# Optimization experiments

Measured on AMD Instinct MI355X. Metric: run time of the kernel, lower is better.

Reference implementation:

```python
import jax, jax.numpy as jnp
import numpy as np

V = 12000; WE = 1000; FEAT = 2048; FE = 1024; H = 1024; AH = 512; NREG = 36; B = 128; T = 17
PAD_ID = 0


def _lstm_cell(x, h, c, wih, whh, bih, bhh):
    # torch LSTMCell: gates ordered (input, forget, cell, output)
    g = x @ wih.T + h @ whh.T + bih + bhh
    i, f, gg, o = jnp.split(g, 4, axis=-1)
    c_new = jax.nn.sigmoid(f) * c + jax.nn.sigmoid(i) * jnp.tanh(gg)
    h_new = jax.nn.sigmoid(o) * jnp.tanh(c_new)
    return h_new, c_new


def setup_inputs() -> dict:
    key = jax.random.key(0)
    ks = jax.random.split(key, 24)
    s = 0.02
    emb_w = jax.random.normal(ks[0], (V, WE), jnp.float32) * s
    emb_w = emb_w.at[PAD_ID].set(0.0)  # padding_idx row is zero
    inp = {
        'fc_feats': jax.random.normal(ks[1], (B, FEAT), jnp.float32),
        'att_feats': jax.random.normal(ks[2], (B, NREG, FEAT), jnp.float32),
        'captions': jax.random.randint(ks[3], (B, T), 0, V, jnp.int64),
        'emb_w': emb_w,
        'fc_w': jax.random.normal(ks[4], (FEAT, FE), jnp.float32) * s,
        'fc_b': jnp.zeros((FE,), jnp.float32),
        'atte_w': jax.random.normal(ks[5], (FEAT, FE), jnp.float32) * s,
        'atte_b': jnp.zeros((FE,), jnp.float32),
        'ctx_w': jax.random.normal(ks[6], (FE, AH), jnp.float32) * s,
        'ctx_b': jnp.zeros((AH,), jnp.float32),
        'attl_wih': jax.random.normal(ks[7], (4 * H, H + FE + WE), jnp.float32) * s,
        'attl_whh': jax.random.normal(ks[8], (4 * H, H), jnp.float32) * s,
        'attl_bih': jnp.zeros((4 * H,), jnp.float32),
        'attl_bhh': jnp.zeros((4 * H,), jnp.float32),
        'h2att_w': jax.random.normal(ks[9], (H, AH), jnp.float32) * s,
        'h2att_b': jnp.zeros((AH,), jnp.float32),
        'alpha_w': jax.random.normal(ks[10], (AH,), jnp.float32) * s,
        'alpha_b': jnp.zeros((), jnp.float32),
        'langl_wih': jax.random.normal(ks[11], (4 * H, FE + H), jnp.float32) * s,
        'langl_whh': jax.random.normal(ks[12], (4 * H, H), jnp.float32) * s,
        'langl_bih': jnp.zeros((4 * H,), jnp.float32),
        'langl_bhh': jnp.zeros((4 * H,), jnp.float32),
        'cls_w': jax.random.normal(ks[13], (H, V), jnp.float32) * s,
        'cls_b': jnp.zeros((V,), jnp.float32),
    }
    return inp


def _forward(fc_feats, att_feats, captions, emb_w, fc_w, fc_b, atte_w, atte_b,
             ctx_w, ctx_b, attl_wih, attl_whh, attl_bih, attl_bhh,
             h2att_w, h2att_b, alpha_w, alpha_b,
             langl_wih, langl_whh, langl_bih, langl_bhh, cls_w, cls_b):
    # _prepare_features (eval mode: dropout is identity)
    fc_e = jax.nn.relu(fc_feats @ fc_w + fc_b)                 # [B, FE]
    att_e = jax.nn.relu(att_feats @ atte_w + atte_b)           # [B, N, FE]
    p_att = att_e @ ctx_w + ctx_b                              # [B, N, AH]
    bsz = fc_feats.shape[0]
    h0 = jnp.zeros((bsz, H), fc_feats.dtype)

    def step(carry, it):
        h_att, c_att, h_lang, c_lang = carry
        w = jax.nn.relu(emb_w[it])                             # [B, WE]
        x_att = jnp.concatenate([h_lang, fc_e, w], axis=1)
        h_att, c_att = _lstm_cell(x_att, h_att, c_att, attl_wih, attl_whh, attl_bih, attl_bhh)
        # Attention
        hq = h_att @ h2att_w + h2att_b                          # [B, AH]
        e = jnp.tanh(p_att + hq[:, None, :]) @ alpha_w + alpha_b  # [B, N]
        alpha = jax.nn.softmax(e, axis=1)
        att_res = jnp.einsum('bn,bnd->bd', alpha, att_e)        # [B, FE]
        x_lang = jnp.concatenate([att_res, h_att], axis=1)
        h_lang, c_lang = _lstm_cell(x_lang, h_lang, c_lang, langl_wih, langl_whh, langl_bih, langl_bhh)
        logprobs = jax.nn.log_softmax(h_lang @ cls_w + cls_b, axis=1)  # [B, V]
        return (h_att, c_att, h_lang, c_lang), logprobs

    its = captions[:, :-1].T  # [T-1, B]
    _, outs = jax.lax.scan(step, (h0, h0, h0, h0), its)
    return jnp.transpose(outs, (1, 0, 2))  # [B, T-1, V]


def reference(fc_feats, att_feats, captions, emb_w, fc_w, fc_b, atte_w, atte_b,
              ctx_w, ctx_b, attl_wih, attl_whh, attl_bih, attl_bhh,
              h2att_w, h2att_b, alpha_w, alpha_b,
              langl_wih, langl_whh, langl_bih, langl_bhh, cls_w, cls_b):
    return _forward(fc_feats, att_feats, captions, emb_w, fc_w, fc_b, atte_w, atte_b,
                    ctx_w, ctx_b, attl_wih, attl_whh, attl_bih, attl_bhh,
                    h2att_w, h2att_b, alpha_w, alpha_b,
                    langl_wih, langl_whh, langl_bih, langl_bhh, cls_w, cls_b)
```

## Files before the change

### kernel.cpp

```cpp
#include <hip/hip_runtime.h>
#include <cstddef>
#include <cstdint>

constexpr int CV    = 12000;
constexpr int CVP2  = 12288;
constexpr int CWE   = 1000;
constexpr int CFEAT = 2048;
constexpr int CFE   = 1024;
constexpr int CH    = 1024;
constexpr int CAH   = 512;
constexpr int CNREG = 36;
constexpr int CB    = 128;
constexpr int CT    = 17;
constexpr int G4    = 4096;
constexpr int XH    = 2048;
constexpr int XL3   = 3072;

#define CDIV(a,b) (((a)+(b)-1)/(b))

typedef __bf16 bf16_t;
typedef __bf16 bf16x8 __attribute__((ext_vector_type(8)));
typedef __bf16 bf16x4 __attribute__((ext_vector_type(4)));
typedef float  f32x4  __attribute__((ext_vector_type(4)));

typedef __attribute__((address_space(3))) uint32_t lds_u32;
typedef const __attribute__((address_space(1))) uint32_t glb_u32;

struct Seg { const bf16_t* A; const bf16_t* W; int lda, ldw, kt; };

template<bool RELU, bool OUTBF, int SWZ>
__global__ __launch_bounds__(256)
void pre_gemm(Seg s0, int inner, const float* __restrict__ bias1,
              void* __restrict__ Cout, int ldc)
{
    const int tid = threadIdx.x;
    const int wid = tid >> 6, lane = tid & 63;
    const int wr = wid >> 1, wc = wid & 1;
    const int llo = lane & 15, lhi = lane >> 4;
    const int nb = gridDim.x, id = blockIdx.x;
    const int sw = (id & 7) * (nb >> 3) + (id >> 3);
    int m0, n0;
    if (SWZ == 1)      { n0 = (sw / inner) * 64;  m0 = (sw % inner) * 128; }
    else if (SWZ == 2) { m0 = (sw / inner) * 128; n0 = (sw % inner) * 64;  }
    else {
        const int xcd = id & 7, idx = id >> 3;
        m0 = (((xcd >> 2) << 3) + (idx & 7)) * 128;
        n0 = (((xcd & 3) << 4) + (idx >> 3)) * 64;
    }

    __shared__ __align__(16) uint8_t smA[2][8192];
    __shared__ __align__(16) uint8_t smB[2][4096];

    const int TT = s0.kt;
    f32x4 acc[4][2] = {};

    const int scq = (lane & 3) ^ ((lane >> 3) & 3);
    auto stage = [&](int buf, int ti) {
        const int k0 = ti << 5;
        #pragma unroll
        for (int i = 0; i < 2; ++i) {
            const int cq = wid * 64 + lane + i * 256;
            const int row = cq >> 2;
            const bf16_t* ga = s0.A + (size_t)(m0 + row) * s0.lda + k0 + scq * 8;
            __builtin_amdgcn_global_load_lds((glb_u32*)ga,
                (lds_u32*)(smA[buf] + (wid * 64 + i * 256) * 16 + lane * 16), 16, 0, 0);
        }
        {
            const int row = tid >> 2;
            const bf16_t* gb = s0.W + (size_t)(n0 + row) * s0.ldw + k0 + scq * 8;
            __builtin_amdgcn_global_load_lds((glb_u32*)gb,
                (lds_u32*)(smB[buf] + wid * 1024 + lane * 16), 16, 0, 0);
        }
    };
    auto compute = [&](int buf) {
        bf16x8 af[4], bg[2];
        #pragma unroll
        for (int fm = 0; fm < 4; ++fm) {
            const int r = wr * 64 + fm * 16 + llo;
            const int p = lhi ^ ((r >> 1) & 3);
            af[fm] = *(const bf16x8*)(smA[buf] + r * 64 + p * 16);
        }
        #pragma unroll
        for (int fn = 0; fn < 2; ++fn) {
            const int r = wc * 32 + fn * 16 + llo;
            const int p = lhi ^ ((r >> 1) & 3);
            bg[fn] = *(const bf16x8*)(smB[buf] + r * 64 + p * 16);
        }
        #pragma unroll
        for (int fm = 0; fm < 4; ++fm)
            #pragma unroll
            for (int fn = 0; fn < 2; ++fn)
                acc[fm][fn] = __builtin_amdgcn_mfma_f32_16x16x32_bf16(
                    af[fm], bg[fn], acc[fm][fn], 0, 0, 0);
    };

    stage(0, 0);
    __syncthreads();
    int cur = 0;
    for (int ti = 0; ti < TT; ++ti) {
        if (ti + 1 < TT) stage(cur ^ 1, ti + 1);
        compute(cur);
        __syncthreads();
        cur ^= 1;
    }

    if (OUTBF) {
        bf16_t* st = (bf16_t*)smA;
        #pragma unroll
        for (int fn = 0; fn < 2; ++fn) {
            const int lcol = wc * 32 + fn * 16 + llo;
            const float b = bias1 ? bias1[n0 + lcol] : 0.f;
            #pragma unroll
            for (int fm = 0; fm < 4; ++fm)
                #pragma unroll
                for (int r = 0; r < 4; ++r) {
                    float v = acc[fm][fn][r] + b;
                    if (RELU) v = fmaxf(v, 0.f);
                    st[(wr * 64 + fm * 16 + lhi * 4 + r) * 64 + lcol] = (bf16_t)v;
                }
        }
        __syncthreads();
        #pragma unroll
        for (int i = 0; i < 4; ++i) {
            const int q = tid + i * 256;
            const int row = q >> 3, ch = q & 7;
            *(uint4*)((bf16_t*)Cout + (size_t)(m0 + row) * ldc + n0 + ch * 8)
                = *(const uint4*)&st[row * 64 + ch * 8];
        }
    } else {
        const int colb = n0 + wc * 32;
        const int rowb = m0 + wr * 64 + lhi * 4;
        #pragma unroll
        for (int fn = 0; fn < 2; ++fn) {
            const int col = colb + fn * 16 + llo;
            const float b = bias1 ? bias1[col] : 0.f;
            #pragma unroll
            for (int fm = 0; fm < 4; ++fm)
                #pragma unroll
                for (int r = 0; r < 4; ++r) {
                    float v = acc[fm][fn][r] + b;
                    if (RELU) v = fmaxf(v, 0.f);
                    ((float*)Cout)[(size_t)(rowb + fm * 16 + r) * ldc + col] = v;
                }
        }
    }
}

__global__ __launch_bounds__(256)
void cls_gemm(const bf16_t* __restrict__ A, const bf16_t* __restrict__ W,
              const float* __restrict__ bias, bf16_t* __restrict__ Cout)
{
    const int tid = threadIdx.x;
    const int wid = tid >> 6, lane = tid & 63;
    const int wr = wid >> 1, wc = wid & 1;
    const int llo = lane & 15, lhi = lane >> 4;
    const int id = blockIdx.x;
    const int xcd = id & 7, idx = id >> 3;
    const int mg = xcd & 1, ng = xcd >> 1;
    const int m0 = (mg * 8 + (idx & 7)) * 128;
    const int n0 = (ng * 24 + (idx >> 3)) * 128;

    __shared__ __align__(16) uint8_t smA[2][8192];
    __shared__ __align__(16) uint8_t smB[2][8192];

    constexpr int TT = 32;
    f32x4 acc[4][4] = {};

    const int scq = (lane & 3) ^ ((lane >> 3) & 3);
    auto stage = [&](int buf, int ti) {
        const int k0 = ti << 5;
        #pragma unroll
        for (int i = 0; i < 2; ++i) {
            const int cq = wid * 64 + lane + i * 256;
            const int row = cq >> 2;
            const bf16_t* ga = A + (size_t)(m0 + row) * CH + k0 + scq * 8;
            __builtin_amdgcn_global_load_lds((glb_u32*)ga,
                (lds_u32*)(smA[buf] + (wid * 64 + i * 256) * 16 + lane * 16), 16, 0, 0);
            const bf16_t* gb = W + (size_t)(n0 + row) * CH + k0 + scq * 8;
            __builtin_amdgcn_global_load_lds((glb_u32*)gb,
                (lds_u32*)(smB[buf] + (wid * 64 + i * 256) * 16 + lane * 16), 16, 0, 0);
        }
    };
    auto compute = [&](int buf) {
        bf16x8 af[4], bg[4];
        #pragma unroll
        for (int fm = 0; fm < 4; ++fm) {
            const int r = wr * 64 + fm * 16 + llo;
            const int p = lhi ^ ((r >> 1) & 3);
            af[fm] = *(const bf16x8*)(smA[buf] + r * 64 + p * 16);
        }
        #pragma unroll
        for (int fn = 0; fn < 4; ++fn) {
            const int r = wc * 64 + fn * 16 + llo;
            const int p = lhi ^ ((r >> 1) & 3);
            bg[fn] = *(const bf16x8*)(smB[buf] + r * 64 + p * 16);
        }
        #pragma unroll
        for (int fm = 0; fm < 4; ++fm)
            #pragma unroll
            for (int fn = 0; fn < 4; ++fn)
                acc[fm][fn] = __builtin_amdgcn_mfma_f32_16x16x32_bf16(
                    af[fm], bg[fn], acc[fm][fn], 0, 0, 0);
    };

    stage(0, 0);
    __syncthreads();
    int cur = 0;
    for (int ti = 0; ti < TT; ++ti) {
        if (ti + 1 < TT) stage(cur ^ 1, ti + 1);
        compute(cur);
        __syncthreads();
        cur ^= 1;
    }

    bf16_t* st = (bf16_t*)smA;
    #pragma unroll
    for (int fn = 0; fn < 4; ++fn) {
        const int lcol = wc * 64 + fn * 16 + llo;
        const int col = n0 + lcol;
        const float b = (col < CV) ? bias[col] : 0.f;
        #pragma unroll
        for (int fm = 0; fm < 4; ++fm)
            #pragma unroll
            for (int r = 0; r < 4; ++r)
                st[(wr * 64 + fm * 16 + lhi * 4 + r) * 128 + lcol]
                    = (bf16_t)(acc[fm][fn][r] + b);
    }
    __syncthreads();
    #pragma unroll
    for (int i = 0; i < 8; ++i) {
        const int q = tid + i * 256;
        const int row = q >> 4, ch = q & 15;
        *(uint4*)(Cout + (size_t)(m0 + row) * CVP2 + n0 + ch * 8)
            = *(const uint4*)&st[row * 128 + ch * 8];
    }
}

template<int TAG>
__global__ __launch_bounds__(256)
void gate_split(const bf16_t* __restrict__ A, int lda,
                const bf16_t* __restrict__ W, int ldw, int ktz,
                bf16_t* __restrict__ gpart)
{
    const int tid = threadIdx.x;
    const int w = tid >> 6, lane = tid & 63;
    const int llo = lane & 15, lhi = lane >> 4;
    const int n0 = blockIdx.x * 16;
    const int z  = blockIdx.y;
    const int kb = z * ktz;

    __shared__ __align__(16) uint8_t smA[2][16384];
    __shared__ __align__(16) uint8_t smB[2][2048];

    f32x4 acc0 = {0.f,0.f,0.f,0.f}, acc1 = {0.f,0.f,0.f,0.f};

    const int arow = tid >> 3, ac = tid & 7;
    const int asc = ac ^ (arow & 7);
    const int wvoff = (tid >> 6) * 1024;

    auto stage = [&](int buf, int ti) {
        const int k0 = (kb + ti) << 6;
        #pragma unroll
        for (int i = 0; i < 4; ++i) {
            const bf16_t* gp = A + (size_t)(arow + i * 32) * lda + k0 + asc * 8;
            __builtin_amdgcn_global_load_lds((glb_u32*)gp,
                (lds_u32*)(smA[buf] + i * 4096 + wvoff), 16, 0, 0);
        }
        if (tid < 128) {
            const int brow = tid >> 3, bc = tid & 7;
            const int bsc = bc ^ (brow & 7);
            const bf16_t* gp = W + (size_t)(n0 + brow) * ldw + k0 + bsc * 8;
            __builtin_amdgcn_global_load_lds((glb_u32*)gp,
                (lds_u32*)(smB[buf] + wvoff), 16, 0, 0);
        }
    };
    auto compute = [&](int buf) {
        const int r7 = llo & 7;
        #pragma unroll
        for (int kk = 0; kk < 2; ++kk) {
            const int coff = ((kk * 4 + lhi) ^ r7) << 4;
            bf16x8 a0 = *(const bf16x8*)(smA[buf] + (w * 32 + llo) * 128 + coff);
            bf16x8 a1 = *(const bf16x8*)(smA[buf] + (w * 32 + 16 + llo) * 128 + coff);
            bf16x8 bb = *(const bf16x8*)(smB[buf] + llo * 128 + coff);
            acc0 = __builtin_amdgcn_mfma_f32_16x16x32_bf16(a0, bb, acc0, 0, 0, 0);
            acc1 = __builtin_amdgcn_mfma_f32_16x16x32_bf16(a1, bb, acc1, 0, 0, 0);
        }
    };

    stage(0, 0);
    __syncthreads();
    int cur = 0;
    for (int ti = 0; ti < ktz; ++ti) {
        if (ti + 1 < ktz) stage(cur ^ 1, ti + 1);
        compute(cur);
        __syncthreads();
        cur ^= 1;
    }

    bf16_t* gp = gpart + (size_t)z * CB * G4;
    const int col = n0 + llo;
    #pragma unroll
    for (int r = 0; r < 4; ++r) {
        gp[(size_t)(w * 32 + lhi * 4 + r) * G4 + col] = (bf16_t)acc0[r];
        gp[(size_t)(w * 32 + 16 + lhi * 4 + r) * G4 + col] = (bf16_t)acc1[r];
    }
}

__global__ __launch_bounds__(1024)
void lstm_attn(const bf16_t* __restrict__ gpart, const bf16_t* __restrict__ gpre_fc,
               const bf16_t* __restrict__ gemb,
               const float* __restrict__ cbias, float* __restrict__ c_att,
               const bf16_t* __restrict__ p_att, const bf16_t* __restrict__ att_e,
               const bf16_t* __restrict__ h2att_wT, const float* __restrict__ h2att_b,
               const float* __restrict__ alpha_w, const float* __restrict__ alpha_b,
               bf16_t* __restrict__ xh_nxt, bf16_t* __restrict__ xl_cur)
{
    __shared__ float sh[CH];
    __shared__ float shq[CAH];
    __shared__ float se[64], salpha[64];
    const int b = blockIdx.x, tid = threadIdx.x;

    {
        const int j = tid;
        float g0 = 0.f, g1 = 0.f, g2 = 0.f, g3 = 0.f;
        #pragma unroll
        for (int z = 0; z < 4; ++z) {
            bf16x4 g = *(const bf16x4*)(gpart + (size_t)z * CB * G4 + (size_t)b * G4 + 4 * j);
            g0 += (float)g[0]; g1 += (float)g[1]; g2 += (float)g[2]; g3 += (float)g[3];
        }
        f32x4 cb = *(const f32x4*)(cbias + 4 * j);
        bf16x4 gf4 = *(const bf16x4*)(gpre_fc + (size_t)b * G4 + 4 * j);
        bf16x4 ge4 = *(const bf16x4*)(gemb + (size_t)b * G4 + 4 * j);
        const float gi = g0 + cb[0] + (float)gf4[0] + (float)ge4[0];
        const float gf = g1 + cb[1] + (float)gf4[1] + (float)ge4[1];
        const float gg = g2 + cb[2] + (float)gf4[2] + (float)ge4[2];
        const float go = g3 + cb[3] + (float)gf4[3] + (float)ge4[3];
        const float si = 1.f / (1.f + expf(-gi));
        const float sf = 1.f / (1.f + expf(-gf));
        const float so = 1.f / (1.f + expf(-go));
        const float cn = sf * c_att[b * CH + j] + si * tanhf(gg);
        const float hn = so * tanhf(cn);
        c_att[b * CH + j] = cn;
        sh[j] = hn;
        const bf16_t hb = (bf16_t)hn;
        xh_nxt[(size_t)b * XH + 1024 + j] = hb;
        xl_cur[(size_t)b * XL3 + 1024 + j] = hb;
    }
    __syncthreads();

    {
        const int q2 = tid & 1, n = tid >> 1;
        const bf16_t* wrow = h2att_wT + (size_t)n * CH + q2 * 512;
        float s = 0.f;
        #pragma unroll 4
        for (int k = 0; k < 512; k += 8) {
            bf16x8 w8 = *(const bf16x8*)(wrow + k);
            #pragma unroll
            for (int j = 0; j < 8; ++j) s = fmaf((float)w8[j], sh[q2 * 512 + k + j], s);
        }
        s += __shfl_xor(s, 1);
        if (q2 == 0) shq[n] = s + h2att_b[n];
    }
    __syncthreads();

    {
        const int wave = tid >> 6, lane = tid & 63;
        for (int n = wave; n < CNREG; n += 16) {
            const bf16_t* pr = p_att + ((size_t)b * CNREG + n) * CAH;
            float s = 0.f;
            #pragma unroll
            for (int q = 0; q < CAH / 64; ++q) {
                const int d = lane + q * 64;
                s += alpha_w[d] * tanhf((float)pr[d] + shq[d]);
            }
            for (int off = 32; off; off >>= 1) s += __shfl_down(s, off);
            if (lane == 0) se[n] = s + alpha_b[0];
        }
    }
    __syncthreads();

    {
        float mx = -1e30f;
        for (int n = 0; n < CNREG; ++n) mx = fmaxf(mx, se[n]);
        float sum = 0.f;
        for (int n = 0; n < CNREG; ++n) sum += expf(se[n] - mx);
        if (tid < CNREG) salpha[tid] = expf(se[tid] - mx) / sum;
    }
    __syncthreads();

    {
        const int d = tid;
        float s = 0.f;
        const bf16_t* ae = att_e + (size_t)b * CNREG * CFE + d;
        #pragma unroll 4
        for (int n = 0; n < CNREG; ++n)
            s = fmaf(salpha[n], (float)ae[(size_t)n * CFE], s);
        xl_cur[(size_t)b * XL3 + d] = (bf16_t)s;
    }
}

__global__ __launch_bounds__(256)
void lstm_flat(const bf16_t* __restrict__ gpart, const float* __restrict__ cbias,
               float* __restrict__ c,
               bf16_t* __restrict__ xh_nxt, bf16_t* __restrict__ xl_nxt,
               bf16_t* __restrict__ h_all, int t)
{
    const int idx = blockIdx.x * 256 + threadIdx.x;
    const int b = idx >> 10, j = idx & 1023;
    float g0 = 0.f, g1 = 0.f, g2 = 0.f, g3 = 0.f;
    #pragma unroll
    for (int z = 0; z < 4; ++z) {
        bf16x4 g = *(const bf16x4*)(gpart + (size_t)z * CB * G4 + (size_t)b * G4 + 4 * j);
        g0 += (float)g[0]; g1 += (float)g[1]; g2 += (float)g[2]; g3 += (float)g[3];
    }
    f32x4 cb = *(const f32x4*)(cbias + 4 * j);
    const float si = 1.f / (1.f + expf(-(g0 + cb[0])));
    const float sf = 1.f / (1.f + expf(-(g1 + cb[1])));
    const float so = 1.f / (1.f + expf(-(g3 + cb[3])));
    const float cn = sf * c[idx] + si * tanhf(g2 + cb[2]);
    const float hn = so * tanhf(cn);
    c[idx] = cn;
    const bf16_t hb = (bf16_t)hn;
    xh_nxt[(size_t)b * XH + j] = hb;
    xl_nxt[(size_t)b * XL3 + 2048 + j] = hb;
    h_all[((size_t)b * (CT - 1) + t) * CH + j] = hb;
}

__global__ void convert_pad(const float* __restrict__ src, bf16_t* __restrict__ dst,
                            int C, int Cp)
{
    const int r = blockIdx.y;
    const int c = blockIdx.x * 256 + threadIdx.x;
    if (c >= Cp) return;
    dst[(size_t)r * Cp + c] = (c < C) ? (bf16_t)src[(size_t)r * C + c] : (bf16_t)0.f;
}

__global__ void convert_perm(const float* __restrict__ src, int srcld, int scol0,
                             int valid, bf16_t* __restrict__ dst, int dstld, int dcol0,
                             int ncols)
{
    const int rp = blockIdx.y;
    const int c = blockIdx.x * 256 + threadIdx.x;
    if (c >= ncols) return;
    const int rs = (rp & 3) * 1024 + (rp >> 2);
    const float v = (c < valid) ? src[(size_t)rs * srcld + scol0 + c] : 0.f;
    dst[(size_t)rp * dstld + dcol0 + c] = (bf16_t)v;
}

__global__ void bias_perm(const float* __restrict__ bih, const float* __restrict__ bhh,
                          float* __restrict__ dst)
{
    const int rp = blockIdx.x * 256 + threadIdx.x;
    if (rp >= G4) return;
    const int rs = (rp & 3) * 1024 + (rp >> 2);
    dst[rp] = bih[rs] + bhh[rs];
}

__global__ __launch_bounds__(256)
void transpose_convert(const float* __restrict__ src, bf16_t* __restrict__ dst,
                       int K, int N)
{
    __shared__ float tile[32][33];
    const int n0 = blockIdx.x * 32, k0 = blockIdx.y * 32;
    const int tx = threadIdx.x & 31, ty = threadIdx.x >> 5;
    #pragma unroll
    for (int i = 0; i < 4; ++i) {
        const int k = k0 + ty + i * 8, n = n0 + tx;
        tile[ty + i * 8][tx] = (k < K && n < N) ? src[(size_t)k * N + n] : 0.f;
    }
    __syncthreads();
    #pragma unroll
    for (int i = 0; i < 4; ++i) {
        const int n = n0 + ty + i * 8, k = k0 + tx;
        if (n < N && k < K) dst[(size_t)n * K + k] = (bf16_t)tile[tx][ty + i * 8];
    }
}

__global__ void emb_all(const float* __restrict__ emb_w,
                        const int* __restrict__ captions, bf16_t* __restrict__ w_emb)
{
    const int r = blockIdx.y;
    const int j = blockIdx.x * 256 + threadIdx.x;
    const int t = r >> 7, b = r & 127;
    const int tok = captions[b * CT + t];
    const float v = (j < CWE) ? fmaxf(emb_w[(size_t)tok * CWE + j], 0.f) : 0.f;
    w_emb[(size_t)r * 1024 + j] = (bf16_t)v;
}

__global__ __launch_bounds__(256)
void logsoftmax_bf(const bf16_t* __restrict__ lg, float* __restrict__ out)
{
    __shared__ float red[4];
    const int r = blockIdx.x, tid = threadIdx.x;
    const bf16_t* row = lg + (size_t)r * CVP2;

    float v[48];
    float mx = -1e30f;
    #pragma unroll
    for (int i = 0; i < 6; ++i) {
        const int c = tid + i * 256;
        if (c < 1500) {
            bf16x8 x = *(const bf16x8*)(row + c * 8);
            #pragma unroll
            for (int j = 0; j < 8; ++j) {
                v[i * 8 + j] = (float)x[j];
                mx = fmaxf(mx, v[i * 8 + j]);
            }
        } else {
            #pragma unroll
            for (int j = 0; j < 8; ++j) v[i * 8 + j] = -1e30f;
        }
    }
    for (int off = 32; off; off >>= 1) mx = fmaxf(mx, __shfl_down(mx, off));
    if ((tid & 63) == 0) red[tid >> 6] = mx;
    __syncthreads();
    mx = fmaxf(fmaxf(red[0], red[1]), fmaxf(red[2], red[3]));
    __syncthreads();

    float sum = 0.f;
    #pragma unroll
    for (int i = 0; i < 6; ++i)
        if (tid + i * 256 < 1500)
            #pragma unroll
            for (int j = 0; j < 8; ++j) sum += expf(v[i * 8 + j] - mx);
    for (int off = 32; off; off >>= 1) sum += __shfl_down(sum, off);
    if ((tid & 63) == 0) red[tid >> 6] = sum;
    __syncthreads();
    sum = red[0] + red[1] + red[2] + red[3];
    const float lse = mx + logf(sum);

    #pragma unroll
    for (int i = 0; i < 6; ++i) {
        const int c = tid + i * 256;
        if (c < 1500) {
            float* o = out + (size_t)r * CV + c * 8;
            float4 a = make_float4(v[i*8+0]-lse, v[i*8+1]-lse, v[i*8+2]-lse, v[i*8+3]-lse);
            float4 bq = make_float4(v[i*8+4]-lse, v[i*8+5]-lse, v[i*8+6]-lse, v[i*8+7]-lse);
            *(float4*)o = a;
            *(float4*)(o + 4) = bq;
        }
    }
}

extern "C" void kernel_launch(void* const* d_in, const int* in_sizes, int n_in,
                              void* d_out, int out_size, void* d_ws, size_t ws_size,
                              hipStream_t stream)
{
    const float* fc_feats  = (const float*)d_in[0];
    const float* att_feats = (const float*)d_in[1];
    const int*   captions  = (const int*)  d_in[2];
    const float* emb_w     = (const float*)d_in[3];
    const float* fc_w      = (const float*)d_in[4];
    const float* fc_b      = (const float*)d_in[5];
    const float* atte_w    = (const float*)d_in[6];
    const float* atte_b    = (const float*)d_in[7];
    const float* ctx_w     = (const float*)d_in[8];
    const float* ctx_b     = (const float*)d_in[9];
    const float* attl_wih  = (const float*)d_in[10];
    const float* attl_whh  = (const float*)d_in[11];
    const float* attl_bih  = (const float*)d_in[12];
    const float* attl_bhh  = (const float*)d_in[13];
    const float* h2att_w   = (const float*)d_in[14];
    const float* h2att_b   = (const float*)d_in[15];
    const float* alpha_w   = (const float*)d_in[16];
    const float* alpha_b   = (const float*)d_in[17];
    const float* langl_wih = (const float*)d_in[18];
    const float* langl_whh = (const float*)d_in[19];
    const float* langl_bih = (const float*)d_in[20];
    const float* langl_bhh = (const float*)d_in[21];
    const float* cls_w     = (const float*)d_in[22];
    const float* cls_b     = (const float*)d_in[23];

    float* out = (float*)d_out;

    char* p = (char*)d_ws;
    auto alloc_bf = [&](size_t e) { bf16_t* q = (bf16_t*)p; p += e * 2; return q; };
    auto alloc_f  = [&](size_t e) { float*  q = (float*) p; p += e * 4; return q; };

    bf16_t* Wcat_att    = alloc_bf((size_t)G4 * XH);
    bf16_t* Wcat_lang   = alloc_bf((size_t)G4 * XL3);
    bf16_t* Win_fc      = alloc_bf((size_t)G4 * 1024);
    bf16_t* Win_emb     = alloc_bf((size_t)G4 * 1024);
    bf16_t* fc_wT_b     = alloc_bf((size_t)CFE * CFEAT);
    bf16_t* atte_wT_b   = alloc_bf((size_t)CFE * CFEAT);
    bf16_t* ctx_wT_b    = alloc_bf((size_t)CAH * CFE);
    bf16_t* h2att_wT_b  = alloc_bf((size_t)CAH * CH);
    bf16_t* cls_wT_b    = alloc_bf((size_t)CVP2 * CH);
    bf16_t* fc_feats_b  = alloc_bf((size_t)CB * CFEAT);
    bf16_t* att_feats_b = alloc_bf((size_t)CB * CNREG * CFEAT);
    bf16_t* att_e_b     = alloc_bf((size_t)CB * CNREG * CFE);
    bf16_t* w_emb       = alloc_bf((size_t)(CT - 1) * CB * 1024);
    bf16_t* fc_e_b      = alloc_bf((size_t)CB * CFE);
    bf16_t* gpre_fc     = alloc_bf((size_t)CB * G4);
    bf16_t* xh0         = alloc_bf((size_t)CB * XH);
    bf16_t* xh1         = alloc_bf((size_t)CB * XH);
    bf16_t* xl3a        = alloc_bf((size_t)CB * XL3);
    bf16_t* xl3b        = alloc_bf((size_t)CB * XL3);
    bf16_t* h_all       = alloc_bf((size_t)CB * (CT - 1) * CH);
    bf16_t* p_att       = alloc_bf((size_t)CB * CNREG * CAH);
    bf16_t* gpart       = alloc_bf((size_t)4 * CB * G4);
    float*  cbias_att   = alloc_f (G4);
    float*  cbias_lang  = alloc_f (G4);
    float*  c_att       = alloc_f ((size_t)CB * CH);
    float*  c_lang      = alloc_f ((size_t)CB * CH);

    bf16_t* Gemb   = att_feats_b;
    bf16_t* logits = Wcat_att;

    hipMemsetAsync(xh0,    0, (size_t)CB * XH * 2, stream);
    hipMemsetAsync(xh1,    0, (size_t)CB * XH * 2, stream);
    hipMemsetAsync(xl3a,   0, (size_t)CB * XL3 * 2, stream);
    hipMemsetAsync(xl3b,   0, (size_t)CB * XL3 * 2, stream);
    hipMemsetAsync(c_att,  0, (size_t)CB * CH * 4, stream);
    hipMemsetAsync(c_lang, 0, (size_t)CB * CH * 4, stream);
    hipMemsetAsync(cls_wT_b + (size_t)CV * CH, 0, (size_t)(CVP2 - CV) * CH * 2, stream);

    const dim3 blk(256);
    auto mk = [](const bf16_t* A, int lda, const bf16_t* W, int ldw, int kt) {
        return Seg{A, W, lda, ldw, kt};
    };

    convert_perm<<<dim3(4, G4), blk, 0, stream>>>(attl_wih, 3048, 0, 1024, Wcat_att, XH, 0, 1024);
    convert_perm<<<dim3(4, G4), blk, 0, stream>>>(attl_whh, 1024, 0, 1024, Wcat_att, XH, 1024, 1024);
    convert_perm<<<dim3(4, G4), blk, 0, stream>>>(attl_wih, 3048, 1024, 1024, Win_fc, 1024, 0, 1024);
    convert_perm<<<dim3(4, G4), blk, 0, stream>>>(attl_wih, 3048, 2048, 1000, Win_emb, 1024, 0, 1024);
    convert_perm<<<dim3(8, G4), blk, 0, stream>>>(langl_wih, 2048, 0, 2048, Wcat_lang, XL3, 0, 2048);
    convert_perm<<<dim3(4, G4), blk, 0, stream>>>(langl_whh, 1024, 0, 1024, Wcat_lang, XL3, 2048, 1024);
    bias_perm<<<16, blk, 0, stream>>>(attl_bih, attl_bhh, cbias_att);
    bias_perm<<<16, blk, 0, stream>>>(langl_bih, langl_bhh, cbias_lang);
    convert_pad<<<dim3(8, CB), blk, 0, stream>>>(fc_feats, fc_feats_b, CFEAT, CFEAT);
    convert_pad<<<dim3(8, CB * CNREG), blk, 0, stream>>>(att_feats, att_feats_b, CFEAT, CFEAT);
    transpose_convert<<<dim3(CFE/32, CFEAT/32), blk, 0, stream>>>(fc_w,    fc_wT_b,    CFEAT, CFE);
    transpose_convert<<<dim3(CFE/32, CFEAT/32), blk, 0, stream>>>(atte_w,  atte_wT_b,  CFEAT, CFE);
    transpose_convert<<<dim3(CAH/32, CFE/32),   blk, 0, stream>>>(ctx_w,   ctx_wT_b,   CFE,   CAH);
    transpose_convert<<<dim3(CAH/32, CH/32),    blk, 0, stream>>>(h2att_w, h2att_wT_b, CH,    CAH);
    transpose_convert<<<dim3(CDIV(CV,32), CH/32), blk, 0, stream>>>(cls_w, cls_wT_b,   CH,    CV);
    emb_all<<<dim3(4, (CT - 1) * CB), blk, 0, stream>>>(emb_w, captions, w_emb);

    pre_gemm<true,true,2><<<16, blk, 0, stream>>>(
        mk(fc_feats_b, CFEAT, fc_wT_b, CFEAT, 64), 16, fc_b, fc_e_b, CFE);
    pre_gemm<true,true,2><<<576, blk, 0, stream>>>(
        mk(att_feats_b, CFEAT, atte_wT_b, CFEAT, 64), 16, atte_b, att_e_b, CFE);
    pre_gemm<false,true,2><<<288, blk, 0, stream>>>(
        mk(att_e_b, CFE, ctx_wT_b, CFE, 32), 8, ctx_b, p_att, CAH);
    pre_gemm<false,true,1><<<64, blk, 0, stream>>>(
        mk(fc_e_b, CFE, Win_fc, 1024, 32), 1, nullptr, gpre_fc, G4);
    pre_gemm<false,true,3><<<1024, blk, 0, stream>>>(
        mk(w_emb, 1024, Win_emb, 1024, 32), 0, nullptr, Gemb, G4);

    for (int t = 0; t < CT - 1; ++t) {
        bf16_t* xh_cur = (t & 1) ? xh1 : xh0;
        bf16_t* xh_nxt = (t & 1) ? xh0 : xh1;
        bf16_t* xl_cur = (t & 1) ? xl3b : xl3a;
        bf16_t* xl_nxt = (t & 1) ? xl3a : xl3b;

        gate_split<0><<<dim3(256, 4), blk, 0, stream>>>(
            xh_cur, XH, Wcat_att, XH, 8, gpart);

        lstm_attn<<<CB, dim3(1024), 0, stream>>>(
            gpart, gpre_fc, Gemb + (size_t)t * CB * G4, cbias_att, c_att,
            p_att, att_e_b, h2att_wT_b, h2att_b, alpha_w, alpha_b,
            xh_nxt, xl_cur);

        gate_split<1><<<dim3(256, 4), blk, 0, stream>>>(
            xl_cur, XL3, Wcat_lang, XL3, 12, gpart);

        lstm_flat<<<512, blk, 0, stream>>>(
            gpart, cbias_lang, c_lang, xh_nxt, xl_nxt, h_all, t);
    }

    cls_gemm<<<1536, blk, 0, stream>>>(h_all, cls_wT_b, cls_b, logits);
    logsoftmax_bf<<<2048, blk, 0, stream>>>(logits, out);
}
```

Measured before the change: 1.575 ms.

## Fuse split-K gate GEMM with LSTM cell update via in-block K reduction

Result: slower. 1.802 ms (+14.5%).

```diff
diff --git a/kernel.cpp b/kernel.cpp
--- a/kernel.cpp
+++ b/kernel.cpp
@@ -236,116 +236,123 @@
     }
 }
 
-template<int TAG>
-__global__ __launch_bounds__(256)
-void gate_split(const bf16_t* __restrict__ A, int lda,
-                const bf16_t* __restrict__ W, int ldw, int ktz,
-                bf16_t* __restrict__ gpart)
+template<int MODE>
+__global__ __launch_bounds__(1024)
+void gate_full(const bf16_t* __restrict__ A, int lda,
+               const bf16_t* __restrict__ W, int ldw, int TT,
+               const bf16_t* __restrict__ gpre_fc, const bf16_t* __restrict__ gemb,
+               const float* __restrict__ cbias, float* __restrict__ cstate,
+               bf16_t* __restrict__ h1, int ldh1,
+               bf16_t* __restrict__ h2, int ldh2,
+               bf16_t* __restrict__ h3, int ldh3)
 {
     const int tid = threadIdx.x;
     const int w = tid >> 6, lane = tid & 63;
+    const int kg = w & 3, mg = w >> 2;
     const int llo = lane & 15, lhi = lane >> 4;
     const int n0 = blockIdx.x * 16;
-    const int z  = blockIdx.y;
-    const int kb = z * ktz;
-
-    __shared__ __align__(16) uint8_t smA[2][16384];
-    __shared__ __align__(16) uint8_t smB[2][2048];
+    const int kb = kg * TT;
+
+    __shared__ __align__(16) uint8_t pool[98304];
+    uint8_t* wbase = pool + w * 6144;
 
     f32x4 acc0 = {0.f,0.f,0.f,0.f}, acc1 = {0.f,0.f,0.f,0.f};
 
-    const int arow = tid >> 3, ac = tid & 7;
-    const int asc = ac ^ (arow & 7);
-    const int wvoff = (tid >> 6) * 1024;
-
+    const int scq = (lane & 3) ^ ((lane >> 3) & 3);
     auto stage = [&](int buf, int ti) {
-        const int k0 = (kb + ti) << 6;
-        #pragma unroll
-        for (int i = 0; i < 4; ++i) {
-            const bf16_t* gp = A + (size_t)(arow + i * 32) * lda + k0 + asc * 8;
-            __builtin_amdgcn_global_load_lds((glb_u32*)gp,
-                (lds_u32*)(smA[buf] + i * 4096 + wvoff), 16, 0, 0);
-        }
-        if (tid < 128) {
-            const int brow = tid >> 3, bc = tid & 7;
-            const int bsc = bc ^ (brow & 7);
-            const bf16_t* gp = W + (size_t)(n0 + brow) * ldw + k0 + bsc * 8;
-            __builtin_amdgcn_global_load_lds((glb_u32*)gp,
-                (lds_u32*)(smB[buf] + wvoff), 16, 0, 0);
+        const int k0 = (kb + ti) << 5;
+        #pragma unroll
+        for (int i = 0; i < 2; ++i) {
+            const int cq = lane + i * 64;
+            const int row = cq >> 2;
+            const bf16_t* ga = A + (size_t)(mg * 32 + row) * lda + k0 + scq * 8;
+            __builtin_amdgcn_global_load_lds((glb_u32*)ga,
+                (lds_u32*)(wbase + buf * 2048 + cq * 16), 16, 0, 0);
+        }
+        {
+            const int row = lane >> 2;
+            const bf16_t* gb = W + (size_t)(n0 + row) * ldw + k0 + scq * 8;
+            __builtin_amdgcn_global_load_lds((glb_u32*)gb,
+                (lds_u32*)(wbase + 4096 + buf * 1024 + lane * 16), 16, 0, 0);
         }
     };
     auto compute = [&](int buf) {
-        const int r7 = llo & 7;
-        #pragma unroll
-        for (int kk = 0; kk < 2; ++kk) {
-            const int coff = ((kk * 4 + lhi) ^ r7) << 4;
-            bf16x8 a0 = *(const bf16x8*)(smA[buf] + (w * 32 + llo) * 128 + coff);
-            bf16x8 a1 = *(const bf16x8*)(smA[buf] + (w * 32 + 16 + llo) * 128 + coff);
-            bf16x8 bb = *(const bf16x8*)(smB[buf] + llo * 128 + coff);
-            acc0 = __builtin_amdgcn_mfma_f32_16x16x32_bf16(a0, bb, acc0, 0, 0, 0);
-            acc1 = __builtin_amdgcn_mfma_f32_16x16x32_bf16(a1, bb, acc1, 0, 0, 0);
-        }
+        const int p = lhi ^ ((llo >> 1) & 3);
+        bf16x8 a0 = *(const bf16x8*)(wbase + buf * 2048 + llo * 64 + p * 16);
+        bf16x8 a1 = *(const bf16x8*)(wbase + buf * 2048 + (16 + llo) * 64 + p * 16);
+        bf16x8 bb = *(const bf16x8*)(wbase + 4096 + buf * 1024 + llo * 64 + p * 16);
+        acc0 = __builtin_amdgcn_mfma_f32_16x16x32_bf16(a0, bb, acc0, 0, 0, 0);
+        acc1 = __builtin_amdgcn_mfma_f32_16x16x32_bf16(a1, bb, acc1, 0, 0, 0);
     };
 
     stage(0, 0);
-    __syncthreads();
+    if (TT > 1) stage(1, 1);
     int cur = 0;
-    for (int ti = 0; ti < ktz; ++ti) {
-        if (ti + 1 < ktz) stage(cur ^ 1, ti + 1);
+    for (int ti = 0; ti < TT; ++ti) {
+        if (ti + 1 < TT) asm volatile("s_waitcnt vmcnt(3)" ::: "memory");
+        else             asm volatile("s_waitcnt vmcnt(0)" ::: "memory");
+        __builtin_amdgcn_sched_barrier(0);
         compute(cur);
-        __syncthreads();
+        __builtin_amdgcn_sched_barrier(0);
+        if (ti + 2 < TT) stage(cur, ti + 2);
         cur ^= 1;
     }
 
-    bf16_t* gp = gpart + (size_t)z * CB * G4;
-    const int col = n0 + llo;
+    __syncthreads();
+
+    float* part = (float*)pool;
+    float* pw = part + kg * 2048;
     #pragma unroll
     for (int r = 0; r < 4; ++r) {
-        gp[(size_t)(w * 32 + lhi * 4 + r) * G4 + col] = (bf16_t)acc0[r];
-        gp[(size_t)(w * 32 + 16 + lhi * 4 + r) * G4 + col] = (bf16_t)acc1[r];
+        pw[(mg * 32 + lhi * 4 + r) * 16 + llo] = acc0[r];
+        pw[(mg * 32 + 16 + lhi * 4 + r) * 16 + llo] = acc1[r];
+    }
+    __syncthreads();
+
+    if (tid < 512) {
+        const int b = tid >> 2, u = tid & 3;
+        const int jg = blockIdx.x * 4 + u;
+        f32x4 g = *(const f32x4*)(part + (size_t)b * 16 + u * 4);
+        #pragma unroll
+        for (int z = 1; z < 4; ++z)
+            g += *(const f32x4*)(part + z * 2048 + (size_t)b * 16 + u * 4);
+        g += *(const f32x4*)(cbias + n0 + u * 4);
+        float gi = g[0], gf = g[1], gg = g[2], go = g[3];
+        if (MODE == 0) {
+            bf16x4 gf4 = *(const bf16x4*)(gpre_fc + (size_t)b * G4 + n0 + u * 4);
+            bf16x4 ge4 = *(const bf16x4*)(gemb + (size_t)b * G4 + n0 + u * 4);
+            gi += (float)gf4[0] + (float)ge4[0];
+            gf += (float)gf4[1] + (float)ge4[1];
+            gg += (float)gf4[2] + (float)ge4[2];
+            go += (float)gf4[3] + (float)ge4[3];
+        }
+        const float si = 1.f / (1.f + expf(-gi));
+        const float sf = 1.f / (1.f + expf(-gf));
+        const float so = 1.f / (1.f + expf(-go));
+        const float cold = cstate[b * CH + jg];
+        const float cn = sf * cold + si * tanhf(gg);
+        const float hn = so * tanhf(cn);
+        cstate[b * CH + jg] = cn;
+        const bf16_t hb = (bf16_t)hn;
+        h1[(size_t)b * ldh1 + jg] = hb;
+        if (h2) h2[(size_t)b * ldh2 + jg] = hb;
+        if (h3) h3[(size_t)b * ldh3 + jg] = hb;
     }
 }
 
 __global__ __launch_bounds__(1024)
-void lstm_attn(const bf16_t* __restrict__ gpart, const bf16_t* __restrict__ gpre_fc,
-               const bf16_t* __restrict__ gemb,
-               const float* __restrict__ cbias, float* __restrict__ c_att,
-               const bf16_t* __restrict__ p_att, const bf16_t* __restrict__ att_e,
-               const bf16_t* __restrict__ h2att_wT, const float* __restrict__ h2att_b,
-               const float* __restrict__ alpha_w, const float* __restrict__ alpha_b,
-               bf16_t* __restrict__ xh_nxt, bf16_t* __restrict__ xl_cur)
+void attn_k(const bf16_t* __restrict__ hsrc, int ldh,
+            const bf16_t* __restrict__ p_att, const bf16_t* __restrict__ att_e,
+            const bf16_t* __restrict__ h2att_wT, const float* __restrict__ h2att_b,
+            const float* __restrict__ alpha_w, const float* __restrict__ alpha_b,
+            bf16_t* __restrict__ xl_cur)
 {
     __shared__ float sh[CH];
     __shared__ float shq[CAH];
     __shared__ float se[64], salpha[64];
     const int b = blockIdx.x, tid = threadIdx.x;
 
-    {
-        const int j = tid;
-        float g0 = 0.f, g1 = 0.f, g2 = 0.f, g3 = 0.f;
-        #pragma unroll
-        for (int z = 0; z < 4; ++z) {
-            bf16x4 g = *(const bf16x4*)(gpart + (size_t)z * CB * G4 + (size_t)b * G4 + 4 * j);
-            g0 += (float)g[0]; g1 += (float)g[1]; g2 += (float)g[2]; g3 += (float)g[3];
-        }
-        f32x4 cb = *(const f32x4*)(cbias + 4 * j);
-        bf16x4 gf4 = *(const bf16x4*)(gpre_fc + (size_t)b * G4 + 4 * j);
-        bf16x4 ge4 = *(const bf16x4*)(gemb + (size_t)b * G4 + 4 * j);
-        const float gi = g0 + cb[0] + (float)gf4[0] + (float)ge4[0];
-        const float gf = g1 + cb[1] + (float)gf4[1] + (float)ge4[1];
-        const float gg = g2 + cb[2] + (float)gf4[2] + (float)ge4[2];
-        const float go = g3 + cb[3] + (float)gf4[3] + (float)ge4[3];
-        const float si = 1.f / (1.f + expf(-gi));
-        const float sf = 1.f / (1.f + expf(-gf));
-        const float so = 1.f / (1.f + expf(-go));
-        const float cn = sf * c_att[b * CH + j] + si * tanhf(gg);
-        const float hn = so * tanhf(cn);
-        c_att[b * CH + j] = cn;
-        sh[j] = hn;
-        const bf16_t hb = (bf16_t)hn;
-        xh_nxt[(size_t)b * XH + 1024 + j] = hb;
-        xl_cur[(size_t)b * XL3 + 1024 + j] = hb;
-    }
+    sh[tid] = (float)hsrc[(size_t)b * ldh + tid];
     __syncthreads();
 
     {
@@ -397,33 +404,6 @@
             s = fmaf(salpha[n], (float)ae[(size_t)n * CFE], s);
         xl_cur[(size_t)b * XL3 + d] = (bf16_t)s;
     }
-}
-
-__global__ __launch_bounds__(256)
-void lstm_flat(const bf16_t* __restrict__ gpart, const float* __restrict__ cbias,
-               float* __restrict__ c,
-               bf16_t* __restrict__ xh_nxt, bf16_t* __restrict__ xl_nxt,
-               bf16_t* __restrict__ h_all, int t)
-{
-    const int idx = blockIdx.x * 256 + threadIdx.x;
-    const int b = idx >> 10, j = idx & 1023;
-    float g0 = 0.f, g1 = 0.f, g2 = 0.f, g3 = 0.f;
-    #pragma unroll
-    for (int z = 0; z < 4; ++z) {
-        bf16x4 g = *(const bf16x4*)(gpart + (size_t)z * CB * G4 + (size_t)b * G4 + 4 * j);
-        g0 += (float)g[0]; g1 += (float)g[1]; g2 += (float)g[2]; g3 += (float)g[3];
-    }
-    f32x4 cb = *(const f32x4*)(cbias + 4 * j);
-    const float si = 1.f / (1.f + expf(-(g0 + cb[0])));
-    const float sf = 1.f / (1.f + expf(-(g1 + cb[1])));
-    const float so = 1.f / (1.f + expf(-(g3 + cb[3])));
-    const float cn = sf * c[idx] + si * tanhf(g2 + cb[2]);
-    const float hn = so * tanhf(cn);
-    c[idx] = cn;
-    const bf16_t hb = (bf16_t)hn;
-    xh_nxt[(size_t)b * XH + j] = hb;
-    xl_nxt[(size_t)b * XL3 + 2048 + j] = hb;
-    h_all[((size_t)b * (CT - 1) + t) * CH + j] = hb;
 }
 
 __global__ void convert_pad(const float* __restrict__ src, bf16_t* __restrict__ dst,
@@ -598,7 +578,6 @@
     bf16_t* xl3b        = alloc_bf((size_t)CB * XL3);
     bf16_t* h_all       = alloc_bf((size_t)CB * (CT - 1) * CH);
     bf16_t* p_att       = alloc_bf((size_t)CB * CNREG * CAH);
-    bf16_t* gpart       = alloc_bf((size_t)4 * CB * G4);
     float*  cbias_att   = alloc_f (G4);
     float*  cbias_lang  = alloc_f (G4);
     float*  c_att       = alloc_f ((size_t)CB * CH);
@@ -654,19 +633,25 @@
         bf16_t* xl_cur = (t & 1) ? xl3b : xl3a;
         bf16_t* xl_nxt = (t & 1) ? xl3a : xl3b;
 
-        gate_split<0><<<dim3(256, 4), blk, 0, stream>>>(
-            xh_cur, XH, Wcat_att, XH, 8, gpart);
-
-        lstm_attn<<<CB, dim3(1024), 0, stream>>>(
-            gpart, gpre_fc, Gemb + (size_t)t * CB * G4, cbias_att, c_att,
-            p_att, att_e_b, h2att_wT_b, h2att_b, alpha_w, alpha_b,
-            xh_nxt, xl_cur);
-
-        gate_split<1><<<dim3(256, 4), blk, 0, stream>>>(
-            xl_cur, XL3, Wcat_lang, XL3, 12, gpart);
-
-        lstm_flat<<<512, blk, 0, stream>>>(
-            gpart, cbias_lang, c_lang, xh_nxt, xl_nxt, h_all, t);
+        gate_full<0><<<256, dim3(1024), 0, stream>>>(
+            xh_cur, XH, Wcat_att, XH, 16,
+            gpre_fc, Gemb + (size_t)t * CB * G4,
+            cbias_att, c_att,
+            xh_nxt + 1024, XH,
+            xl_cur + 1024, XL3,
+            nullptr, 0);
+
+        attn_k<<<CB, dim3(1024), 0, stream>>>(
+            xl_cur + 1024, XL3,
+            p_att, att_e_b, h2att_wT_b, h2att_b, alpha_w, alpha_b, xl_cur);
+
+        gate_full<1><<<256, dim3(1024), 0, stream>>>(
+            xl_cur, XL3, Wcat_lang, XL3, 24,
+            nullptr, nullptr,
+            cbias_lang, c_lang,
+            xh_nxt, XH,
+            xl_nxt + 2048, XL3,
+            h_all + (size_t)t * CH, (CT - 1) * CH);
     }
 
     cls_gemm<<<1536, blk, 0, stream>>>(h_all, cls_wT_b, cls_b, logits);
```
